# Performance work log

Hardware: AMD Instinct MI355X
Metric: run time of the kernel (lower is better)

The kernel has to match this reference:

```python
import jax, jax.numpy as jnp
import numpy as np

N_NODES = 100000   # nodes in the sampled subgraph (len(entity))
N_EDGES = 1000000  # edges
DIM = 128          # dim_size
N_REL = 16         # num_relations * 2 (conv is built with doubled relations)
N_ENT = 500000     # num_entities (embedding table rows)


def setup_inputs() -> dict:
    key = jax.random.key(0)
    ks = jax.random.split(key, 9)
    s = 1.0 / np.sqrt(DIM)
    entity = jax.random.randint(ks[0], (N_NODES,), 0, N_ENT)
    edge_index = jax.random.randint(ks[1], (2, N_EDGES), 0, N_NODES)
    edge_type = jax.random.randint(ks[2], (N_EDGES,), 0, N_REL)
    edge_norm = jax.random.normal(ks[3], (N_EDGES,), dtype=jnp.float32)  # unused by the module's math
    emb_table = jax.random.normal(ks[4], (N_ENT, DIM), dtype=jnp.float32)
    W1 = jax.random.normal(ks[5], (N_REL, DIM, DIM), dtype=jnp.float32) * s
    root1 = jax.random.normal(ks[6], (DIM, DIM), dtype=jnp.float32) * s
    W2 = jax.random.normal(ks[7], (N_REL, DIM, DIM), dtype=jnp.float32) * s
    root2 = jax.random.normal(ks[8], (DIM, DIM), dtype=jnp.float32) * s
    return {"entity": entity, "edge_index": edge_index, "edge_type": edge_type,
            "edge_norm": edge_norm, "emb_table": emb_table,
            "W1": W1, "root1": root1, "W2": W2, "root2": root2}


def _rgcn_conv(x, src, dst, edge_type, W_rel, W_root):
    # Relation-routed linear on source features, then scatter-MEAN to dst, plus root linear.
    # Project every node by every relation matrix once (R small), then gather per-edge:
    h_all = jnp.einsum('nd,rdo->rno', x, W_rel)        # [R, N, D]
    msgs = h_all[edge_type, src]                       # [E, D] per-edge messages
    n = x.shape[0]
    agg = jax.ops.segment_sum(msgs, dst, num_segments=n)
    cnt = jax.ops.segment_sum(jnp.ones(src.shape, x.dtype), dst, num_segments=n)
    agg = agg / jnp.maximum(cnt, 1.0)[:, None]         # mean; zero-degree nodes stay 0 (PyG semantics)
    return agg + x @ W_root


def reference(entity, edge_index, edge_type, edge_norm, emb_table, W1, root1, W2, root2):
    src, dst = edge_index[0], edge_index[1]
    x = emb_table[entity]                              # nn.Embedding lookup
    x = jax.nn.relu(_rgcn_conv(x, src, dst, edge_type, W1, root1))
    # dropout is identity in eval mode
    x = _rgcn_conv(x, src, dst, edge_type, W2, root2)
    return x
```

## Files before the change

kernel.cpp:

```cpp
#include <hip/hip_runtime.h>
#include <hip/hip_bf16.h>
#include <stdint.h>

#define D     128
#define DPAD  136
#define TM    64
#define NB    256
#define RMAX  64
#define SCAN_T 1024

typedef __bf16 bf16_t;
typedef __bf16 bf16x8 __attribute__((ext_vector_type(8)));
typedef float  f32x4  __attribute__((ext_vector_type(4)));


__global__ void deg_kernel(const int* __restrict__ ei, int E, int* __restrict__ cnt) {
    int e = blockIdx.x * blockDim.x + threadIdx.x;
    if (e < E) atomicAdd(&cnt[ei[E + e]], 1);
}

__global__ void inv_kernel(const int* __restrict__ cnt, float* __restrict__ inv, int N) {
    int n = blockIdx.x * blockDim.x + threadIdx.x;
    if (n < N) inv[n] = 1.0f / (float)max(cnt[n], 1);
}

__global__ void hist_kernel(const int* __restrict__ et, int E, int chunk,
                            int R, int* __restrict__ blockhist) {
    __shared__ int h[RMAX];
    int tid = threadIdx.x;
    if (tid < R) h[tid] = 0;
    __syncthreads();
    int start = blockIdx.x * chunk;
    int end   = min(E, start + chunk);
    for (int i = start + tid; i < end; i += blockDim.x)
        atomicAdd(&h[et[i]], 1);
    __syncthreads();
    if (tid < R) blockhist[blockIdx.x * R + tid] = h[tid];
}

__global__ void scan_kernel(int* __restrict__ blockhist, int R,
                            int* __restrict__ blockoff,
                            int* __restrict__ rel_off, int* __restrict__ tile_base,
                            int* __restrict__ tile_rel, int* __restrict__ tile_idx) {
    __shared__ int tot[RMAX];
    __shared__ int s_off[RMAX + 1], s_tb[RMAX + 1];
    int tid = threadIdx.x;
    if (tid < R) {
        int run = 0;
        for (int b = 0; b < NB; b++) run += blockhist[b * R + tid];
        tot[tid] = run;
    }
    __syncthreads();
    if (tid == 0) {
        int acc = 0, tb = 0;
        for (int r = 0; r < R; r++) {
            s_off[r] = acc; s_tb[r] = tb;
            acc += tot[r];
            tb  += (tot[r] + TM - 1) / TM;
        }
        s_off[R] = acc; s_tb[R] = tb;
    }
    __syncthreads();
    if (tid <= R) {
        rel_off[tid]   = s_off[tid];
        tile_base[tid] = s_tb[tid];
    }
    if (tid < R) {
        int run = s_off[tid];
        for (int b = 0; b < NB; b++) {
            int v = blockhist[b * R + tid];
            blockoff[b * R + tid] = run;
            run += v;
        }
    }
    __syncthreads();
    for (int r = 0; r < R; r++) {
        int nt = s_tb[r + 1] - s_tb[r];
        for (int t = tid; t < nt; t += blockDim.x) {
            tile_rel[s_tb[r] + t] = r;
            tile_idx[s_tb[r] + t] = t;
        }
    }
}

__global__ void scatter2_kernel(const int* __restrict__ ei, const int* __restrict__ et,
                                int E, int chunk, int R,
                                const int* __restrict__ blockoff,
                                int* __restrict__ s_src, int* s_dst, int* s_eid) {
    __shared__ int ofs[RMAX];
    int tid = threadIdx.x;
    if (tid < R) ofs[tid] = blockoff[blockIdx.x * R + tid];
    __syncthreads();
    int start = blockIdx.x * chunk;
    int end   = min(E, start + chunk);
    for (int i = start + tid; i < end; i += blockDim.x) {
        int r = et[i];
        int p = atomicAdd(&ofs[r], 1);
        s_src[p] = ei[i];
        if (s_dst) s_dst[p] = ei[E + i];
        if (s_eid) s_eid[p] = i;
    }
}

__global__ void scanN_kernel(const int* __restrict__ cnt, int N,
                             int* __restrict__ dst_off, int* __restrict__ dst_ptr) {
    __shared__ int ts[SCAN_T];
    int tid = threadIdx.x;
    int chunk = (N + SCAN_T - 1) / SCAN_T;
    int s = tid * chunk, e = min(N, s + chunk);
    int sum = 0;
    for (int i = s; i < e; i++) sum += cnt[i];
    ts[tid] = sum;
    __syncthreads();
    for (int off = 1; off < SCAN_T; off <<= 1) {
        int v = (tid >= off) ? ts[tid - off] : 0;
        __syncthreads();
        ts[tid] += v;
        __syncthreads();
    }
    int run = (tid == 0) ? 0 : ts[tid - 1];
    for (int i = s; i < e; i++) {
        dst_off[i] = run;
        dst_ptr[i] = run;
        run += cnt[i];
    }
    if (tid == SCAN_T - 1) dst_off[N] = run;
}

__global__ void dstclaim_kernel(const int* __restrict__ ei, int E,
                                int* __restrict__ dst_ptr, int* __restrict__ dstpos) {
    int i = blockIdx.x * blockDim.x + threadIdx.x;
    if (i < E) dstpos[i] = atomicAdd(&dst_ptr[ei[E + i]], 1);
}

__global__ void map_kernel(const int* __restrict__ s_eid, const int* __restrict__ dstpos,
                           int E, int* __restrict__ msgpos) {
    int p = blockIdx.x * blockDim.x + threadIdx.x;
    if (p < E) msgpos[p] = dstpos[s_eid[p]];
}

__global__ void transpose_kernel(const float* __restrict__ W1, const float* __restrict__ root1,
                                 const float* __restrict__ W2, const float* __restrict__ root2,
                                 int R, bf16_t* __restrict__ Wt) {
    int m = blockIdx.x;
    const float* src;
    if (m < R)            src = W1 + (size_t)m * D * D;
    else if (m < 2 * R)   src = W2 + (size_t)(m - R) * D * D;
    else if (m == 2 * R)  src = root1;
    else                  src = root2;
    bf16_t* dstp = Wt + (size_t)m * D * D;
    for (int i = threadIdx.x; i < D * D; i += blockDim.x) {
        int o = i >> 7, d = i & 127;
        dstp[i] = (bf16_t)src[d * D + o];
    }
}

__global__ void gather_kernel(const int* __restrict__ entity, const float* __restrict__ emb,
                              bf16_t* __restrict__ x, int N) {
    int t = blockIdx.x * blockDim.x + threadIdx.x;
    if (t >= N * 16) return;
    int n = t >> 4, c = t & 15;
    const float4* src = (const float4*)(emb + (size_t)entity[n] * D) + c * 2;
    float4 a = src[0], b = src[1];
    bf16x8 v = { (bf16_t)a.x, (bf16_t)a.y, (bf16_t)a.z, (bf16_t)a.w,
                 (bf16_t)b.x, (bf16_t)b.y, (bf16_t)b.z, (bf16_t)b.w };
    *(bf16x8*)(x + (size_t)t * 8) = v;
}


__global__ __launch_bounds__(256, 3)
void edge_gemm_scatter(const bf16_t* __restrict__ x, const bf16_t* __restrict__ Wt,
                       const int* __restrict__ s_src_g, const int* __restrict__ msgpos,
                       const int* __restrict__ rel_off, const int* __restrict__ tile_base,
                       const int* __restrict__ tile_rel, const int* __restrict__ tile_idx,
                       int R, bf16_t* __restrict__ msgs) {
    __shared__ bf16_t sW[D * DPAD];
    __shared__ bf16_t sA[TM * DPAD];
    __shared__ int   sh_src[TM];
    __shared__ int   sh_slot[TM];

    int tile = blockIdx.x;
    if (tile >= tile_base[R]) return;
    int r = tile_rel[tile];
    int t = tile_idx[tile];
    int base = rel_off[r] + t * TM;
    int cntE = min(TM, rel_off[r + 1] - base);

    int tid = threadIdx.x;
    if (tid < TM) {
        int ok = tid < cntE;
        sh_src[tid]  = ok ? s_src_g[base + tid] : 0;
        sh_slot[tid] = ok ? msgpos[base + tid] : 0;
    }
    const uint4* Wg = (const uint4*)(Wt + (size_t)r * D * D);
    for (int c = tid; c < D * 16; c += 256) {
        int row = c >> 4, col = c & 15;
        *(uint4*)&sW[row * DPAD + col * 8] = Wg[c];
    }
    __syncthreads();
    for (int c = tid; c < TM * 16; c += 256) {
        int row = c >> 4, col = c & 15;
        const uint4* xr = (const uint4*)(x + (size_t)sh_src[row] * D);
        *(uint4*)&sA[row * DPAD + col * 8] = xr[col];
    }
    __syncthreads();

    int lane = tid & 63;
    int w = tid >> 6;
    int m = lane & 15, q = lane >> 4;
    f32x4 acc[4][2];
#pragma unroll
    for (int a = 0; a < 4; a++)
#pragma unroll
        for (int b = 0; b < 2; b++) acc[a][b] = (f32x4){0.f, 0.f, 0.f, 0.f};

#pragma unroll
    for (int k0 = 0; k0 < D; k0 += 32) {
        bf16x8 af[4], bfr[2];
#pragma unroll
        for (int mt = 0; mt < 4; mt++)
            af[mt] = *(const bf16x8*)&sA[(mt * 16 + m) * DPAD + k0 + q * 8];
#pragma unroll
        for (int nt = 0; nt < 2; nt++)
            bfr[nt] = *(const bf16x8*)&sW[(w * 32 + nt * 16 + m) * DPAD + k0 + q * 8];
#pragma unroll
        for (int mt = 0; mt < 4; mt++)
#pragma unroll
            for (int nt = 0; nt < 2; nt++)
                acc[mt][nt] = __builtin_amdgcn_mfma_f32_16x16x32_bf16(af[mt], bfr[nt], acc[mt][nt], 0, 0, 0);
    }

    __syncthreads();
#pragma unroll
    for (int mt = 0; mt < 4; mt++)
#pragma unroll
        for (int i = 0; i < 4; i++) {
            int row = mt * 16 + q * 4 + i;
#pragma unroll
            for (int nt = 0; nt < 2; nt++)
                sA[row * DPAD + w * 32 + nt * 16 + m] = (bf16_t)acc[mt][nt][i];
        }
    __syncthreads();
    for (int c = tid; c < cntE * 16; c += 256) {
        int row = c >> 4, col = c & 15;
        ((uint4*)msgs)[(size_t)sh_slot[row] * 16 + col] = *(uint4*)&sA[row * DPAD + col * 8];
    }
}

__global__ __launch_bounds__(256, 3)
void edge_gemm_atomic(const bf16_t* __restrict__ x, const bf16_t* __restrict__ Wt,
                      const int* __restrict__ s_src_g, const int* __restrict__ s_dst_g,
                      const float* __restrict__ inv_cnt,
                      const int* __restrict__ rel_off, const int* __restrict__ tile_base,
                      const int* __restrict__ tile_rel, const int* __restrict__ tile_idx,
                      int R, float* __restrict__ agg) {
    __shared__ bf16_t sW[D * DPAD];
    __shared__ bf16_t sA[TM * DPAD];
    __shared__ int   sh_src[TM];
    __shared__ int   sh_dst[TM];
    __shared__ float sh_inv[TM];

    int tile = blockIdx.x;
    if (tile >= tile_base[R]) return;
    int r = tile_rel[tile];
    int t = tile_idx[tile];
    int base = rel_off[r] + t * TM;
    int cntE = min(TM, rel_off[r + 1] - base);

    int tid = threadIdx.x;
    if (tid < TM) {
        int ok = tid < cntE;
        int s  = ok ? s_src_g[base + tid] : 0;
        int dd = ok ? s_dst_g[base + tid] : 0;
        sh_src[tid] = s;
        sh_dst[tid] = dd;
        sh_inv[tid] = ok ? inv_cnt[dd] : 0.f;
    }
    const uint4* Wg = (const uint4*)(Wt + (size_t)r * D * D);
    for (int c = tid; c < D * 16; c += 256) {
        int row = c >> 4, col = c & 15;
        *(uint4*)&sW[row * DPAD + col * 8] = Wg[c];
    }
    __syncthreads();
    for (int c = tid; c < TM * 16; c += 256) {
        int row = c >> 4, col = c & 15;
        const uint4* xr = (const uint4*)(x + (size_t)sh_src[row] * D);
        *(uint4*)&sA[row * DPAD + col * 8] = xr[col];
    }
    __syncthreads();

    int lane = tid & 63;
    int w = tid >> 6;
    int m = lane & 15, q = lane >> 4;
    f32x4 acc[4][2];
#pragma unroll
    for (int a = 0; a < 4; a++)
#pragma unroll
        for (int b = 0; b < 2; b++) acc[a][b] = (f32x4){0.f, 0.f, 0.f, 0.f};

#pragma unroll
    for (int k0 = 0; k0 < D; k0 += 32) {
        bf16x8 af[4], bfr[2];
#pragma unroll
        for (int mt = 0; mt < 4; mt++)
            af[mt] = *(const bf16x8*)&sA[(mt * 16 + m) * DPAD + k0 + q * 8];
#pragma unroll
        for (int nt = 0; nt < 2; nt++)
            bfr[nt] = *(const bf16x8*)&sW[(w * 32 + nt * 16 + m) * DPAD + k0 + q * 8];
#pragma unroll
        for (int mt = 0; mt < 4; mt++)
#pragma unroll
            for (int nt = 0; nt < 2; nt++)
                acc[mt][nt] = __builtin_amdgcn_mfma_f32_16x16x32_bf16(af[mt], bfr[nt], acc[mt][nt], 0, 0, 0);
    }

#pragma unroll
    for (int mt = 0; mt < 4; mt++)
#pragma unroll
        for (int i = 0; i < 4; i++) {
            int edge = mt * 16 + q * 4 + i;
            if (edge < cntE) {
                float sc = sh_inv[edge];
                float* ag = agg + (size_t)sh_dst[edge] * D;
#pragma unroll
                for (int nt = 0; nt < 2; nt++) {
                    int o = w * 32 + nt * 16 + m;
                    atomicAdd(&ag[o], acc[mt][nt][i] * sc);
                }
            }
        }
}

__global__ __launch_bounds__(256)
void seg_sum(const bf16_t* __restrict__ msgs, const int* __restrict__ dst_off,
             const float* __restrict__ inv, float* __restrict__ agg, int N) {
    int node = blockIdx.x * 16 + (threadIdx.x >> 4);
    int t = threadIdx.x & 15;
    if (node >= N) return;
    int s = dst_off[node], e = dst_off[node + 1];
    float sum[8] = {0.f, 0.f, 0.f, 0.f, 0.f, 0.f, 0.f, 0.f};
    for (int j = s; j < e; j++) {
        bf16x8 v = *(const bf16x8*)(msgs + (size_t)j * D + t * 8);
#pragma unroll
        for (int k = 0; k < 8; k++) sum[k] += (float)v[k];
    }
    float sc = inv[node];
    float* out = agg + (size_t)node * D + t * 8;
    *(float4*)out       = (float4){sum[0] * sc, sum[1] * sc, sum[2] * sc, sum[3] * sc};
    *(float4*)(out + 4) = (float4){sum[4] * sc, sum[5] * sc, sum[6] * sc, sum[7] * sc};
}

__global__ __launch_bounds__(256, 3)
void root_gemm(const bf16_t* x, const bf16_t* __restrict__ roott,
               const float* __restrict__ agg, bf16_t* out16, float* out32,
               int N, int relu) {
    __shared__ bf16_t sW[D * DPAD];
    __shared__ bf16_t sA[TM * DPAD];
    int tid = threadIdx.x;
    int nbase = blockIdx.x * TM;

    const uint4* Wg = (const uint4*)roott;
    for (int c = tid; c < D * 16; c += 256) {
        int row = c >> 4, col = c & 15;
        *(uint4*)&sW[row * DPAD + col * 8] = Wg[c];
    }
    for (int c = tid; c < TM * 16; c += 256) {
        int row = c >> 4, col = c & 15;
        int n = nbase + row;
        if (n >= N) n = N - 1;
        *(uint4*)&sA[row * DPAD + col * 8] = ((const uint4*)(x + (size_t)n * D))[col];
    }
    __syncthreads();

    int lane = tid & 63;
    int w = tid >> 6;
    int m = lane & 15, q = lane >> 4;
    f32x4 acc[4][2];
#pragma unroll
    for (int a = 0; a < 4; a++)
#pragma unroll
        for (int b = 0; b < 2; b++) acc[a][b] = (f32x4){0.f, 0.f, 0.f, 0.f};

#pragma unroll
    for (int k0 = 0; k0 < D; k0 += 32) {
        bf16x8 af[4], bfr[2];
#pragma unroll
        for (int mt = 0; mt < 4; mt++)
            af[mt] = *(const bf16x8*)&sA[(mt * 16 + m) * DPAD + k0 + q * 8];
#pragma unroll
        for (int nt = 0; nt < 2; nt++)
            bfr[nt] = *(const bf16x8*)&sW[(w * 32 + nt * 16 + m) * DPAD + k0 + q * 8];
#pragma unroll
        for (int mt = 0; mt < 4; mt++)
#pragma unroll
            for (int nt = 0; nt < 2; nt++)
                acc[mt][nt] = __builtin_amdgcn_mfma_f32_16x16x32_bf16(af[mt], bfr[nt], acc[mt][nt], 0, 0, 0);
    }

#pragma unroll
    for (int mt = 0; mt < 4; mt++)
#pragma unroll
        for (int i = 0; i < 4; i++) {
            int row = mt * 16 + q * 4 + i;
            int n = nbase + row;
            if (n < N) {
#pragma unroll
                for (int nt = 0; nt < 2; nt++) {
                    int o = w * 32 + nt * 16 + m;
                    float v = acc[mt][nt][i] + agg[(size_t)n * D + o];
                    if (relu) v = fmaxf(v, 0.f);
                    if (out16) out16[(size_t)n * D + o] = (bf16_t)v;
                    else       out32[(size_t)n * D + o] = v;
                }
            }
        }
}


extern "C" void kernel_launch(void* const* d_in, const int* in_sizes, int n_in,
                              void* d_out, int out_size, void* d_ws, size_t ws_size,
                              hipStream_t stream) {
    const int*   entity = (const int*)d_in[0];
    const int*   ei     = (const int*)d_in[1];
    const int*   et     = (const int*)d_in[2];
    const float* emb    = (const float*)d_in[4];
    const float* W1     = (const float*)d_in[5];
    const float* root1  = (const float*)d_in[6];
    const float* W2     = (const float*)d_in[7];
    const float* root2  = (const float*)d_in[8];

    const int N = in_sizes[0];
    const int E = in_sizes[2];
    const int R = in_sizes[5] / (D * D);

    char* p = (char*)d_ws;
    auto alloc = [&](size_t bytes) -> char* {
        char* q = p; p += (bytes + 255) & ~(size_t)255; return q;
    };
    float*  agg      = (float*)alloc((size_t)N * D * 4);
    bf16_t* x        = (bf16_t*)alloc((size_t)N * D * 2);
    bf16_t* Wt       = (bf16_t*)alloc((size_t)(2 * R + 2) * D * D * 2);
    int*    s_src    = (int*)alloc((size_t)E * 4);
    int*    cnt      = (int*)alloc((size_t)N * 4);
    float*  inv      = (float*)alloc((size_t)N * 4);
    int*    blockhist= (int*)alloc((size_t)NB * R * 4);
    int*    blockoff = (int*)alloc((size_t)NB * R * 4);
    int*    rel_off  = (int*)alloc((size_t)(R + 1) * 4);
    int*    tile_bs  = (int*)alloc((size_t)(R + 1) * 4);
    const int maxtiles = (E + TM - 1) / TM + R;
    int*    tile_rel = (int*)alloc((size_t)maxtiles * 4);
    int*    tile_idx = (int*)alloc((size_t)maxtiles * 4);
    char*   p_common = p;

    bf16_t* msgs    = (bf16_t*)alloc((size_t)E * D * 2);
    int*    s_eid   = (int*)alloc((size_t)E * 4);
    int*    msgpos  = (int*)alloc((size_t)E * 4);
    int*    dstpos  = (int*)alloc((size_t)E * 4);
    int*    dst_off = (int*)alloc((size_t)(N + 1) * 4);
    int*    dst_ptr = (int*)alloc((size_t)N * 4);
    bool big = ((size_t)(p - (char*)d_ws) <= ws_size);

    int* s_dst = nullptr;
    if (!big) { p = p_common; s_dst = (int*)alloc((size_t)E * 4); }

    const int chunk = (E + NB - 1) / NB;

    hipMemsetAsync(cnt, 0, (size_t)N * 4, stream);
    deg_kernel<<<(E + 255) / 256, 256, 0, stream>>>(ei, E, cnt);
    inv_kernel<<<(N + 255) / 256, 256, 0, stream>>>(cnt, inv, N);
    hist_kernel<<<NB, 256, 0, stream>>>(et, E, chunk, R, blockhist);
    scan_kernel<<<1, 256, 0, stream>>>(blockhist, R, blockoff, rel_off, tile_bs, tile_rel, tile_idx);
    scatter2_kernel<<<NB, 256, 0, stream>>>(ei, et, E, chunk, R, blockoff,
                                            s_src, big ? nullptr : s_dst, big ? s_eid : nullptr);
    transpose_kernel<<<2 * R + 2, 256, 0, stream>>>(W1, root1, W2, root2, R, Wt);
    gather_kernel<<<(N * 16 + 255) / 256, 256, 0, stream>>>(entity, emb, x, N);

    if (big) {
        scanN_kernel<<<1, SCAN_T, 0, stream>>>(cnt, N, dst_off, dst_ptr);
        dstclaim_kernel<<<(E + 255) / 256, 256, 0, stream>>>(ei, E, dst_ptr, dstpos);
        map_kernel<<<(E + 255) / 256, 256, 0, stream>>>(s_eid, dstpos, E, msgpos);

        edge_gemm_scatter<<<maxtiles, 256, 0, stream>>>(x, Wt, s_src, msgpos,
                                                        rel_off, tile_bs, tile_rel, tile_idx, R, msgs);
        seg_sum<<<(N + 15) / 16, 256, 0, stream>>>(msgs, dst_off, inv, agg, N);
        root_gemm<<<(N + TM - 1) / TM, 256, 0, stream>>>(x, Wt + (size_t)(2 * R) * D * D, agg,
                                                         x, (float*)nullptr, N, 1);
        edge_gemm_scatter<<<maxtiles, 256, 0, stream>>>(x, Wt + (size_t)R * D * D, s_src, msgpos,
                                                        rel_off, tile_bs, tile_rel, tile_idx, R, msgs);
        seg_sum<<<(N + 15) / 16, 256, 0, stream>>>(msgs, dst_off, inv, agg, N);
        root_gemm<<<(N + TM - 1) / TM, 256, 0, stream>>>(x, Wt + (size_t)(2 * R + 1) * D * D, agg,
                                                         (bf16_t*)nullptr, (float*)d_out, N, 0);
    } else {
        hipMemsetAsync(agg, 0, (size_t)N * D * 4, stream);
        edge_gemm_atomic<<<maxtiles, 256, 0, stream>>>(x, Wt, s_src, s_dst, inv,
                                                       rel_off, tile_bs, tile_rel, tile_idx, R, agg);
        root_gemm<<<(N + TM - 1) / TM, 256, 0, stream>>>(x, Wt + (size_t)(2 * R) * D * D, agg,
                                                         x, (float*)nullptr, N, 1);
        hipMemsetAsync(agg, 0, (size_t)N * D * 4, stream);
        edge_gemm_atomic<<<maxtiles, 256, 0, stream>>>(x, Wt + (size_t)R * D * D, s_src, s_dst, inv,
                                                       rel_off, tile_bs, tile_rel, tile_idx, R, agg);
        root_gemm<<<(N + TM - 1) / TM, 256, 0, stream>>>(x, Wt + (size_t)(2 * R + 1) * D * D, agg,
                                                         (bf16_t*)nullptr, (float*)d_out, N, 0);
    }
}
```

Before: 1.164 ms.

## Parallelize node-degree scan, fuse edge-position mapping, stage block histograms in LDS

The single-block N-element prefix scan becomes a three-kernel multi-block scan (per-block sums, a scan of those sums, then per-block writes), so it no longer serialises on one workgroup. scatter2 now records each edge's relation-sorted position, which lets dstclaim write msgpos directly. That removes map_kernel along with its s_eid and dstpos round trip. The relation scan kernel also stages the block histogram in shared memory, transposed, before its serial per-relation loops. The cost is two extra launches for the scan and scattered writes into msgpos.

```diff
diff --git a/kernel.cpp b/kernel.cpp
--- a/kernel.cpp
+++ b/kernel.cpp
@@ -7,7 +7,9 @@
 #define TM    64
 #define NB    256
 #define RMAX  64
-#define SCAN_T 1024
+#define RS    16
+#define NSB   128
+#define NST   256
 
 typedef __bf16 bf16_t;
 typedef __bf16 bf16x8 __attribute__((ext_vector_type(8)));
@@ -42,12 +44,22 @@
                             int* __restrict__ blockoff,
                             int* __restrict__ rel_off, int* __restrict__ tile_base,
                             int* __restrict__ tile_rel, int* __restrict__ tile_idx) {
+    __shared__ int s_bh[NB * RS];
     __shared__ int tot[RMAX];
     __shared__ int s_off[RMAX + 1], s_tb[RMAX + 1];
     int tid = threadIdx.x;
+    const bool staged = (R <= RS);
+    if (staged) {
+        for (int i = tid; i < NB * R; i += blockDim.x) {
+            int b = i / R, r = i - b * R;
+            s_bh[r * NB + b] = blockhist[i];
+        }
+    }
+    __syncthreads();
     if (tid < R) {
         int run = 0;
-        for (int b = 0; b < NB; b++) run += blockhist[b * R + tid];
+        if (staged) { for (int b = 0; b < NB; b++) run += s_bh[tid * NB + b]; }
+        else        { for (int b = 0; b < NB; b++) run += blockhist[b * R + tid]; }
         tot[tid] = run;
     }
     __syncthreads();
@@ -68,7 +80,7 @@
     if (tid < R) {
         int run = s_off[tid];
         for (int b = 0; b < NB; b++) {
-            int v = blockhist[b * R + tid];
+            int v = staged ? s_bh[tid * NB + b] : blockhist[b * R + tid];
             blockoff[b * R + tid] = run;
             run += v;
         }
@@ -86,7 +98,7 @@
 __global__ void scatter2_kernel(const int* __restrict__ ei, const int* __restrict__ et,
                                 int E, int chunk, int R,
                                 const int* __restrict__ blockoff,
-                                int* __restrict__ s_src, int* s_dst, int* s_eid) {
+                                int* __restrict__ s_src, int* s_dst, int* relpos) {
     __shared__ int ofs[RMAX];
     int tid = threadIdx.x;
     if (tid < R) ofs[tid] = blockoff[blockIdx.x * R + tid];
@@ -98,45 +110,82 @@
         int p = atomicAdd(&ofs[r], 1);
         s_src[p] = ei[i];
         if (s_dst) s_dst[p] = ei[E + i];
-        if (s_eid) s_eid[p] = i;
-    }
-}
-
-__global__ void scanN_kernel(const int* __restrict__ cnt, int N,
-                             int* __restrict__ dst_off, int* __restrict__ dst_ptr) {
-    __shared__ int ts[SCAN_T];
-    int tid = threadIdx.x;
-    int chunk = (N + SCAN_T - 1) / SCAN_T;
-    int s = tid * chunk, e = min(N, s + chunk);
+        if (relpos) relpos[i] = p;
+    }
+}
+
+
+__global__ void nsum_kernel(const int* __restrict__ cnt, int N, int chunkN,
+                            int* __restrict__ bsum) {
+    __shared__ int red[NST];
+    int b = blockIdx.x, tid = threadIdx.x;
+    int s = b * chunkN, e = min(N, s + chunkN);
     int sum = 0;
-    for (int i = s; i < e; i++) sum += cnt[i];
-    ts[tid] = sum;
-    __syncthreads();
-    for (int off = 1; off < SCAN_T; off <<= 1) {
-        int v = (tid >= off) ? ts[tid - off] : 0;
+    for (int i = s + tid; i < e; i += NST) sum += cnt[i];
+    red[tid] = sum;
+    __syncthreads();
+    for (int off = NST / 2; off > 0; off >>= 1) {
+        if (tid < off) red[tid] += red[tid + off];
         __syncthreads();
-        ts[tid] += v;
+    }
+    if (tid == 0) bsum[b] = red[0];
+}
+
+__global__ void nscanB_kernel(int* __restrict__ bsum, int nb) {
+    __shared__ int ts[NST];
+    int tid = threadIdx.x;
+    int v = (tid < nb) ? bsum[tid] : 0;
+    ts[tid] = v;
+    __syncthreads();
+    for (int off = 1; off < NST; off <<= 1) {
+        int t = (tid >= off) ? ts[tid - off] : 0;
         __syncthreads();
-    }
-    int run = (tid == 0) ? 0 : ts[tid - 1];
-    for (int i = s; i < e; i++) {
-        dst_off[i] = run;
-        dst_ptr[i] = run;
-        run += cnt[i];
-    }
-    if (tid == SCAN_T - 1) dst_off[N] = run;
+        ts[tid] += t;
+        __syncthreads();
+    }
+    if (tid < nb) bsum[tid] = ts[tid] - v;
+    if (tid == nb - 1) bsum[nb] = ts[tid];
+}
+
+__global__ void nwrite_kernel(const int* __restrict__ cnt, int N, int chunkN,
+                              const int* __restrict__ bsum,
+                              int* __restrict__ dst_off, int* __restrict__ dst_ptr) {
+    __shared__ int tile[NST];
+    __shared__ int carry;
+    int b = blockIdx.x, tid = threadIdx.x;
+    int s = b * chunkN, e = min(N, s + chunkN);
+    if (tid == 0) carry = bsum[b];
+    __syncthreads();
+    for (int base = s; base < e; base += NST) {
+        int i = base + tid;
+        int v = (i < e) ? cnt[i] : 0;
+        tile[tid] = v;
+        __syncthreads();
+        for (int off = 1; off < NST; off <<= 1) {
+            int t = (tid >= off) ? tile[tid - off] : 0;
+            __syncthreads();
+            tile[tid] += t;
+            __syncthreads();
+        }
+        int incl = tile[tid];
+        int excl = carry + incl - v;
+        if (i < e) { dst_off[i] = excl; dst_ptr[i] = excl; }
+        __syncthreads();
+        if (tid == 0) carry += tile[NST - 1];
+        __syncthreads();
+    }
+    if (b == 0 && tid == 0) dst_off[N] = bsum[NSB];
 }
 
 __global__ void dstclaim_kernel(const int* __restrict__ ei, int E,
-                                int* __restrict__ dst_ptr, int* __restrict__ dstpos) {
+                                int* __restrict__ dst_ptr,
+                                const int* __restrict__ relpos,
+                                int* __restrict__ msgpos) {
     int i = blockIdx.x * blockDim.x + threadIdx.x;
-    if (i < E) dstpos[i] = atomicAdd(&dst_ptr[ei[E + i]], 1);
-}
-
-__global__ void map_kernel(const int* __restrict__ s_eid, const int* __restrict__ dstpos,
-                           int E, int* __restrict__ msgpos) {
-    int p = blockIdx.x * blockDim.x + threadIdx.x;
-    if (p < E) msgpos[p] = dstpos[s_eid[p]];
+    if (i < E) {
+        int p = atomicAdd(&dst_ptr[ei[E + i]], 1);
+        msgpos[relpos[i]] = p;
+    }
 }
 
 __global__ void transpose_kernel(const float* __restrict__ W1, const float* __restrict__ root1,
@@ -453,11 +502,11 @@
     char*   p_common = p;
 
     bf16_t* msgs    = (bf16_t*)alloc((size_t)E * D * 2);
-    int*    s_eid   = (int*)alloc((size_t)E * 4);
+    int*    relpos  = (int*)alloc((size_t)E * 4);
     int*    msgpos  = (int*)alloc((size_t)E * 4);
-    int*    dstpos  = (int*)alloc((size_t)E * 4);
     int*    dst_off = (int*)alloc((size_t)(N + 1) * 4);
     int*    dst_ptr = (int*)alloc((size_t)N * 4);
+    int*    bsum    = (int*)alloc((size_t)(NSB + 1) * 4);
     bool big = ((size_t)(p - (char*)d_ws) <= ws_size);
 
     int* s_dst = nullptr;
@@ -471,14 +520,16 @@
     hist_kernel<<<NB, 256, 0, stream>>>(et, E, chunk, R, blockhist);
     scan_kernel<<<1, 256, 0, stream>>>(blockhist, R, blockoff, rel_off, tile_bs, tile_rel, tile_idx);
     scatter2_kernel<<<NB, 256, 0, stream>>>(ei, et, E, chunk, R, blockoff,
-                                            s_src, big ? nullptr : s_dst, big ? s_eid : nullptr);
+                                            s_src, big ? nullptr : s_dst, big ? relpos : nullptr);
     transpose_kernel<<<2 * R + 2, 256, 0, stream>>>(W1, root1, W2, root2, R, Wt);
     gather_kernel<<<(N * 16 + 255) / 256, 256, 0, stream>>>(entity, emb, x, N);
 
     if (big) {
-        scanN_kernel<<<1, SCAN_T, 0, stream>>>(cnt, N, dst_off, dst_ptr);
-        dstclaim_kernel<<<(E + 255) / 256, 256, 0, stream>>>(ei, E, dst_ptr, dstpos);
-        map_kernel<<<(E + 255) / 256, 256, 0, stream>>>(s_eid, dstpos, E, msgpos);
+        const int chunkN = (N + NSB - 1) / NSB;
+        nsum_kernel<<<NSB, NST, 0, stream>>>(cnt, N, chunkN, bsum);
+        nscanB_kernel<<<1, NST, 0, stream>>>(bsum, NSB);
+        nwrite_kernel<<<NSB, NST, 0, stream>>>(cnt, N, chunkN, bsum, dst_off, dst_ptr);
+        dstclaim_kernel<<<(E + 255) / 256, 256, 0, stream>>>(ei, E, dst_ptr, relpos, msgpos);
 
         edge_gemm_scatter<<<maxtiles, 256, 0, stream>>>(x, Wt, s_src, msgpos,
                                                         rel_off, tile_bs, tile_rel, tile_idx, R, msgs);
```

Measured after the change: 963.6 us. -17.2%, faster.
